# Kernel tuning notes

Hardware: AMD Instinct MI355X
Metric: run time of the kernel (lower is better)

The kernel has to match this reference:

```python
import jax, jax.numpy as jnp
import numpy as np


def _sage_mean_layer(x, src, dst, W_self, W_neigh, b):
    # DGL SAGEConv('mean'): h_neigh = mean_{u in N(v)} x_u ; out = x@W_self + h_neigh@W_neigh + b
    n = x.shape[0]
    msg_sum = jax.ops.segment_sum(x[src], dst, num_segments=n)          # [N, D] scatter-add
    deg = jax.ops.segment_sum(jnp.ones_like(dst, dtype=x.dtype), dst, num_segments=n)
    h_neigh = msg_sum / jnp.maximum(deg, 1.0)[:, None]                   # zero-degree nodes -> 0
    return x @ W_self + h_neigh @ W_neigh + b


def setup_inputs() -> dict:
    key = jax.random.key(0)
    ks = jax.random.split(key, 9)
    N, E, D_in, D_hid, D_out = 50000, 800000, 128, 128, 128
    s = lambda d: 1.0 / np.sqrt(d)
    return {
        "x": jax.random.normal(ks[0], (N, D_in), dtype=jnp.float32),
        "src": jax.random.randint(ks[1], (E,), 0, N, dtype=jnp.int32),
        "dst": jax.random.randint(ks[2], (E,), 0, N, dtype=jnp.int32),
        "W1_self": jax.random.uniform(ks[3], (D_in, D_hid), jnp.float32, -s(D_in), s(D_in)),
        "W1_neigh": jax.random.uniform(ks[4], (D_in, D_hid), jnp.float32, -s(D_in), s(D_in)),
        "b1": jnp.zeros((D_hid,), jnp.float32),
        "W2_self": jax.random.uniform(ks[5], (D_hid, D_out), jnp.float32, -s(D_hid), s(D_hid)),
        "W2_neigh": jax.random.uniform(ks[6], (D_hid, D_out), jnp.float32, -s(D_hid), s(D_hid)),
        "b2": jnp.zeros((D_out,), jnp.float32),
    }


def reference(x, src, dst, W1_self, W1_neigh, b1, W2_self, W2_neigh, b2):
    # layer 1: SAGEConv -> ELU (dropout is identity in eval mode)
    h = jax.nn.elu(_sage_mean_layer(x, src, dst, W1_self, W1_neigh, b1))
    # layer 2: is_out_layer=True -> no activation
    return _sage_mean_layer(h, src, dst, W2_self, W2_neigh, b2)
```

## Files before the change

kernel.cpp:

```cpp
#include <hip/hip_runtime.h>
#include <hip/hip_bf16.h>
#include <math.h>

#define DD 128
#define CAP 64
#define NSHARD 8

typedef __attribute__((ext_vector_type(8))) short short8;
typedef __attribute__((ext_vector_type(4))) float floatx4;
typedef __attribute__((ext_vector_type(8))) unsigned short ushortx8;

__global__ __launch_bounds__(256) void fill_bucket_shard_kernel(
        const int* __restrict__ src, const int* __restrict__ dst,
        int* __restrict__ cnt, int* __restrict__ slot,
        int E, int shard_size, int nchunks) {
    int shard = blockIdx.x & (NSHARD - 1);
    int chunk = blockIdx.x >> 3;
    int lo = shard * shard_size;
    int hi = lo + shard_size;
    int stride = nchunks * 256;
    for (int e = chunk * 256 + threadIdx.x; e < E; e += stride) {
        int d = dst[e];
        if (d >= lo && d < hi) {
            int p = atomicAdd(&cnt[d], 1);
            if (p < CAP) slot[(size_t)d * CAP + p] = src[e];
        }
    }
}


__global__ void cast_bf16_kernel(const float* __restrict__ x, ushort* __restrict__ xb, int n4) {
    int i = blockIdx.x * blockDim.x + threadIdx.x;
    if (i >= n4) return;
    float4 v = *(const float4*)&x[(size_t)i * 4];
    __hip_bfloat16 b0 = __float2bfloat16(v.x), b1 = __float2bfloat16(v.y);
    __hip_bfloat16 b2 = __float2bfloat16(v.z), b3 = __float2bfloat16(v.w);
    ushort4 o;
    o.x = *(ushort*)&b0; o.y = *(ushort*)&b1; o.z = *(ushort*)&b2; o.w = *(ushort*)&b3;
    *(ushort4*)&xb[(size_t)i * 4] = o;
}

__global__ void pack_w_kernel(const float* __restrict__ W1a, const float* __restrict__ W1b,
                              const float* __restrict__ W2a, const float* __restrict__ W2b,
                              ushort* __restrict__ Wp1, ushort* __restrict__ Wp2) {
    int gid = blockIdx.x * blockDim.x + threadIdx.x;
    int layer = gid >> 15;
    int r = gid & 32767;
    int j = r & 7;
    int lane = (r >> 3) & 63;
    int nt = (r >> 9) & 7;
    int ks = r >> 12;
    int k = ks * 32 + (lane >> 4) * 8 + j;
    int col = nt * 16 + (lane & 15);
    const float* W = layer ? (k < 128 ? W2a : W2b) : (k < 128 ? W1a : W1b);
    float v = W[(k & 127) * DD + col];
    __hip_bfloat16 b = __float2bfloat16(v);
    (layer ? Wp2 : Wp1)[r] = *(ushort*)&b;
}

#define BF2F(u) __uint_as_float((unsigned)(u) << 16)

__global__ __launch_bounds__(256) void agg_mean_kernel(
        const ushort* __restrict__ Xb, const int* __restrict__ cnt,
        const int* __restrict__ slot, ushort* __restrict__ Hn, int n) {
    int v = (blockIdx.x * blockDim.x + threadIdx.x) >> 6;
    int lane = threadIdx.x & 63;
    if (v >= n) return;
    int d = cnt[v];
    if (d > CAP) d = CAP;
    int g = lane >> 4;
    int sl = lane & 15;
    int c = sl * 8;

    float acc[8];
#pragma unroll
    for (int j = 0; j < 8; ++j) acc[j] = 0.f;

    if (d > 0) {
        int li = lane < d ? lane : d - 1;
        int idx = slot[(size_t)v * CAP + li];
        int i = 0;
        for (; i + 16 <= d; i += 16) {
            int u0 = __shfl(idx, i + 0 + g);
            int u1 = __shfl(idx, i + 4 + g);
            int u2 = __shfl(idx, i + 8 + g);
            int u3 = __shfl(idx, i + 12 + g);
            ushortx8 y0 = *(const ushortx8*)&Xb[(size_t)u0 * DD + c];
            ushortx8 y1 = *(const ushortx8*)&Xb[(size_t)u1 * DD + c];
            ushortx8 y2 = *(const ushortx8*)&Xb[(size_t)u2 * DD + c];
            ushortx8 y3 = *(const ushortx8*)&Xb[(size_t)u3 * DD + c];
#pragma unroll
            for (int j = 0; j < 8; ++j)
                acc[j] += BF2F((ushort)y0[j]) + BF2F((ushort)y1[j])
                        + BF2F((ushort)y2[j]) + BF2F((ushort)y3[j]);
        }
        for (; i < d; i += 4) {
            int srcl = i + g;
            int valid = srcl < d;
            int u = __shfl(idx, valid ? srcl : (d - 1));
            float w = valid ? 1.f : 0.f;
            ushortx8 y = *(const ushortx8*)&Xb[(size_t)u * DD + c];
#pragma unroll
            for (int j = 0; j < 8; ++j) acc[j] += w * BF2F((ushort)y[j]);
        }
    }

#pragma unroll
    for (int j = 0; j < 8; ++j) {
        acc[j] += __shfl_xor(acc[j], 16);
        acc[j] += __shfl_xor(acc[j], 32);
    }

    if (g == 0) {
        float inv = 1.0f / (float)(d > 0 ? d : 1);
        ushort tmp[8];
#pragma unroll
        for (int j = 0; j < 8; ++j) {
            __hip_bfloat16 b = __float2bfloat16(acc[j] * inv);
            tmp[j] = *(ushort*)&b;
        }
        uint4 ov;
        ov.x = (unsigned)tmp[0] | ((unsigned)tmp[1] << 16);
        ov.y = (unsigned)tmp[2] | ((unsigned)tmp[3] << 16);
        ov.z = (unsigned)tmp[4] | ((unsigned)tmp[5] << 16);
        ov.w = (unsigned)tmp[6] | ((unsigned)tmp[7] << 16);
        *(uint4*)&Hn[(size_t)v * DD + c] = ov;
    }
}

__global__ __launch_bounds__(256) void gemm_fused_kernel(
        const ushort* __restrict__ Xb, const ushort* __restrict__ Hn,
        const ushort* __restrict__ Wp, const float* __restrict__ bias,
        ushort* __restrict__ out_bf16, float* __restrict__ out_f32,
        int nstrips, int do_elu) {
    int strip = blockIdx.x * 4 + (threadIdx.x >> 6);
    if (strip >= nstrips) return;
    int lane = threadIdx.x & 63;
    int m = lane & 15;
    int quad = lane >> 4;
    const size_t row0 = (size_t)strip * 16;
    const ushort* xrow = Xb + (row0 + m) * DD + quad * 8;
    const ushort* hrow = Hn + (row0 + m) * DD + quad * 8;

    floatx4 acc[8];
#pragma unroll
    for (int t = 0; t < 8; ++t) acc[t] = (floatx4){0.f, 0.f, 0.f, 0.f};

#pragma unroll
    for (int ks = 0; ks < 8; ++ks) {
        short8 a = (ks < 4) ? *(const short8*)(xrow + ks * 32)
                            : *(const short8*)(hrow + (ks - 4) * 32);
        const ushort* wp = Wp + ((size_t)(ks * 8) * 64 + lane) * 8;
#pragma unroll
        for (int nt = 0; nt < 8; ++nt) {
            short8 b = *(const short8*)(wp + (size_t)nt * 64 * 8);
            acc[nt] = __builtin_amdgcn_mfma_f32_16x16x32_bf16(a, b, acc[nt], 0, 0, 0);
        }
    }

#pragma unroll
    for (int nt = 0; nt < 8; ++nt) {
        int col = nt * 16 + m;
        float bv = bias[col];
#pragma unroll
        for (int r = 0; r < 4; ++r) {
            size_t row = row0 + quad * 4 + r;
            float v = acc[nt][r] + bv;
            if (do_elu) v = v > 0.f ? v : expm1f(v);
            if (out_f32) {
                out_f32[row * DD + col] = v;
            } else {
                __hip_bfloat16 b = __float2bfloat16(v);
                out_bf16[row * DD + col] = *(ushort*)&b;
            }
        }
    }
}


extern "C" void kernel_launch(void* const* d_in, const int* in_sizes, int n_in,
                              void* d_out, int out_size, void* d_ws, size_t ws_size,
                              hipStream_t stream) {
    const float* x   = (const float*)d_in[0];
    const int*   src = (const int*)d_in[1];
    const int*   dst = (const int*)d_in[2];
    const float* W1s = (const float*)d_in[3];
    const float* W1n = (const float*)d_in[4];
    const float* b1  = (const float*)d_in[5];
    const float* W2s = (const float*)d_in[6];
    const float* W2n = (const float*)d_in[7];
    const float* b2  = (const float*)d_in[8];
    float* out = (float*)d_out;

    const int N = in_sizes[0] / DD;
    const int E = in_sizes[1];

    char* ws = (char*)d_ws;
    int* cnt       = (int*)ws; ws += (size_t)N * 4;
    int* slot      = (int*)ws; ws += (size_t)N * CAP * 4;
    ushort* Wp1    = (ushort*)ws; ws += 65536;
    ushort* Wp2    = (ushort*)ws; ws += 65536;
    ushort* Xb     = (ushort*)ws; ws += (size_t)N * DD * 2;
    ushort* Hn     = (ushort*)ws; ws += (size_t)N * DD * 2;
    ushort* H1     = (ushort*)ws; ws += (size_t)N * DD * 2;

    (void)hipMemsetAsync(cnt, 0, (size_t)N * 4, stream);
    const int shard_size = (N + NSHARD - 1) / NSHARD;
    const int nchunks = 128;
    fill_bucket_shard_kernel<<<nchunks * NSHARD, 256, 0, stream>>>(
        src, dst, cnt, slot, E, shard_size, nchunks);

    cast_bf16_kernel<<<(N * DD / 4 + 255) / 256, 256, 0, stream>>>(x, Xb, N * DD / 4);
    pack_w_kernel<<<256, 256, 0, stream>>>(W1s, W1n, W2s, W2n, Wp1, Wp2);

    const int nstrips = N / 16;
    const int gb = (nstrips + 3) / 4;
    const int ab = (N * 64 + 255) / 256;

    agg_mean_kernel<<<ab, 256, 0, stream>>>(Xb, cnt, slot, Hn, N);
    gemm_fused_kernel<<<gb, 256, 0, stream>>>(Xb, Hn, Wp1, b1, H1, nullptr, nstrips, 1);

    agg_mean_kernel<<<ab, 256, 0, stream>>>(H1, cnt, slot, Hn, N);
    gemm_fused_kernel<<<gb, 256, 0, stream>>>(H1, Hn, Wp2, b2, nullptr, out, nstrips, 0);
}
```

Measured before the change: 242.7 us.

## Fuse bucket fill, bf16 cast and weight pack into one prep kernel

Merges the edge bucketing, the x-to-bf16 cast and the weight packing into a single launch, with block ranges dispatched to each role so the independent work can run concurrently and two launches disappear. The bucket fill now uses more blocks (512 chunks per shard instead of 128) and issues four dst loads per iteration to raise memory-level parallelism. The cast handles 8 elements per thread with 128-bit stores. The trade-off is more blocks scanning all edges with shard filtering, which adds redundant dst reads, and a heterogeneous kernel whose register use is set by the heaviest branch.

```diff
diff --git a/kernel.cpp b/kernel.cpp
--- a/kernel.cpp
+++ b/kernel.cpp
@@ -6,56 +6,92 @@
 #define CAP 64
 #define NSHARD 8
 
+#define FILL_BLOCKS 4096
+#define PACK_BLOCKS 256
+
 typedef __attribute__((ext_vector_type(8))) short short8;
 typedef __attribute__((ext_vector_type(4))) float floatx4;
 typedef __attribute__((ext_vector_type(8))) unsigned short ushortx8;
 
-__global__ __launch_bounds__(256) void fill_bucket_shard_kernel(
+static __device__ __forceinline__ unsigned pack2bf(float a, float b) {
+    __hip_bfloat16 ba = __float2bfloat16(a), bb = __float2bfloat16(b);
+    return (unsigned)*(ushort*)&ba | ((unsigned)*(ushort*)&bb << 16);
+}
+
+__global__ __launch_bounds__(256) void prep_kernel(
+        const float* __restrict__ x,
         const int* __restrict__ src, const int* __restrict__ dst,
         int* __restrict__ cnt, int* __restrict__ slot,
-        int E, int shard_size, int nchunks) {
-    int shard = blockIdx.x & (NSHARD - 1);
-    int chunk = blockIdx.x >> 3;
-    int lo = shard * shard_size;
-    int hi = lo + shard_size;
-    int stride = nchunks * 256;
-    for (int e = chunk * 256 + threadIdx.x; e < E; e += stride) {
-        int d = dst[e];
-        if (d >= lo && d < hi) {
-            int p = atomicAdd(&cnt[d], 1);
-            if (p < CAP) slot[(size_t)d * CAP + p] = src[e];
-        }
-    }
-}
-
-
-__global__ void cast_bf16_kernel(const float* __restrict__ x, ushort* __restrict__ xb, int n4) {
-    int i = blockIdx.x * blockDim.x + threadIdx.x;
-    if (i >= n4) return;
-    float4 v = *(const float4*)&x[(size_t)i * 4];
-    __hip_bfloat16 b0 = __float2bfloat16(v.x), b1 = __float2bfloat16(v.y);
-    __hip_bfloat16 b2 = __float2bfloat16(v.z), b3 = __float2bfloat16(v.w);
-    ushort4 o;
-    o.x = *(ushort*)&b0; o.y = *(ushort*)&b1; o.z = *(ushort*)&b2; o.w = *(ushort*)&b3;
-    *(ushort4*)&xb[(size_t)i * 4] = o;
-}
-
-__global__ void pack_w_kernel(const float* __restrict__ W1a, const float* __restrict__ W1b,
-                              const float* __restrict__ W2a, const float* __restrict__ W2b,
-                              ushort* __restrict__ Wp1, ushort* __restrict__ Wp2) {
-    int gid = blockIdx.x * blockDim.x + threadIdx.x;
-    int layer = gid >> 15;
-    int r = gid & 32767;
-    int j = r & 7;
-    int lane = (r >> 3) & 63;
-    int nt = (r >> 9) & 7;
-    int ks = r >> 12;
-    int k = ks * 32 + (lane >> 4) * 8 + j;
-    int col = nt * 16 + (lane & 15);
-    const float* W = layer ? (k < 128 ? W2a : W2b) : (k < 128 ? W1a : W1b);
-    float v = W[(k & 127) * DD + col];
-    __hip_bfloat16 b = __float2bfloat16(v);
-    (layer ? Wp2 : Wp1)[r] = *(ushort*)&b;
+        const float* __restrict__ W1a, const float* __restrict__ W1b,
+        const float* __restrict__ W2a, const float* __restrict__ W2b,
+        ushort* __restrict__ Wp1, ushort* __restrict__ Wp2,
+        ushort* __restrict__ Xb,
+        int E, int n8, int shard_size, int cast_blocks) {
+    int b = blockIdx.x;
+    if (b < FILL_BLOCKS) {
+        int shard = b & (NSHARD - 1);
+        int chunk = b >> 3;
+        int lo = shard * shard_size;
+        int hi = lo + shard_size;
+        const int stride = (FILL_BLOCKS >> 3) * 256;
+        int e = chunk * 256 + threadIdx.x;
+        for (; e + 3 * stride < E; e += 4 * stride) {
+            int d0 = dst[e];
+            int d1 = dst[e + stride];
+            int d2 = dst[e + 2 * stride];
+            int d3 = dst[e + 3 * stride];
+            if (d0 >= lo && d0 < hi) {
+                int p = atomicAdd(&cnt[d0], 1);
+                if (p < CAP) slot[(size_t)d0 * CAP + p] = src[e];
+            }
+            if (d1 >= lo && d1 < hi) {
+                int p = atomicAdd(&cnt[d1], 1);
+                if (p < CAP) slot[(size_t)d1 * CAP + p] = src[e + stride];
+            }
+            if (d2 >= lo && d2 < hi) {
+                int p = atomicAdd(&cnt[d2], 1);
+                if (p < CAP) slot[(size_t)d2 * CAP + p] = src[e + 2 * stride];
+            }
+            if (d3 >= lo && d3 < hi) {
+                int p = atomicAdd(&cnt[d3], 1);
+                if (p < CAP) slot[(size_t)d3 * CAP + p] = src[e + 3 * stride];
+            }
+        }
+        for (; e < E; e += stride) {
+            int d = dst[e];
+            if (d >= lo && d < hi) {
+                int p = atomicAdd(&cnt[d], 1);
+                if (p < CAP) slot[(size_t)d * CAP + p] = src[e];
+            }
+        }
+    } else if (b < FILL_BLOCKS + cast_blocks) {
+        int i = (b - FILL_BLOCKS) * 256 + threadIdx.x;
+        if (i < n8) {
+            const float4* xp = (const float4*)x;
+            float4 v0 = xp[(size_t)i * 2];
+            float4 v1 = xp[(size_t)i * 2 + 1];
+            uint4 o;
+            o.x = pack2bf(v0.x, v0.y);
+            o.y = pack2bf(v0.z, v0.w);
+            o.z = pack2bf(v1.x, v1.y);
+            o.w = pack2bf(v1.z, v1.w);
+            *(uint4*)&Xb[(size_t)i * 8] = o;
+        }
+    } else {
+        int gid = (b - FILL_BLOCKS - cast_blocks) * 256 + threadIdx.x;
+        int layer = gid >> 15;
+        int r = gid & 32767;
+        int j = r & 7;
+        int lane = (r >> 3) & 63;
+        int nt = (r >> 9) & 7;
+        int ks = r >> 12;
+        int k = ks * 32 + (lane >> 4) * 8 + j;
+        int col = nt * 16 + (lane & 15);
+        const float* W = layer ? (k < 128 ? W2a : W2b) : (k < 128 ? W1a : W1b);
+        float v = W[(k & 127) * DD + col];
+        __hip_bfloat16 bf = __float2bfloat16(v);
+        (layer ? Wp2 : Wp1)[r] = *(ushort*)&bf;
+    }
 }
 
 #define BF2F(u) __uint_as_float((unsigned)(u) << 16)
@@ -205,13 +241,13 @@
     ushort* H1     = (ushort*)ws; ws += (size_t)N * DD * 2;
 
     (void)hipMemsetAsync(cnt, 0, (size_t)N * 4, stream);
+
     const int shard_size = (N + NSHARD - 1) / NSHARD;
-    const int nchunks = 128;
-    fill_bucket_shard_kernel<<<nchunks * NSHARD, 256, 0, stream>>>(
-        src, dst, cnt, slot, E, shard_size, nchunks);
-
-    cast_bf16_kernel<<<(N * DD / 4 + 255) / 256, 256, 0, stream>>>(x, Xb, N * DD / 4);
-    pack_w_kernel<<<256, 256, 0, stream>>>(W1s, W1n, W2s, W2n, Wp1, Wp2);
+    const int n8 = N * DD / 8;
+    const int cast_blocks = (n8 + 255) / 256;
+    prep_kernel<<<FILL_BLOCKS + cast_blocks + PACK_BLOCKS, 256, 0, stream>>>(
+        x, src, dst, cnt, slot, W1s, W1n, W2s, W2n, Wp1, Wp2, Xb,
+        E, n8, shard_size, cast_blocks);
 
     const int nstrips = N / 16;
     const int gb = (nstrips + 3) / 4;
```

New measurement: 235.1 us. 1.03x faster.
